# Kernel optimization log

Hardware: AMD Instinct MI355X
Metric: run time of the kernel (lower is better)

Reference implementation:

```python
import jax, jax.numpy as jnp
import numpy as np

BIG = 1e8  # > max possible squared distance in a 64^3 volume (3*63^2 ~ 1.2e4)


def _edt(mask):
    """Exact Euclidean distance transform (scipy.ndimage.distance_transform_edt).

    mask: [B, X, Y, Z] float; distance at nonzero voxels to nearest zero voxel.
    Uses the exact separable squared-EDT: along each axis,
      g[i] = min_j f[j] + (i - j)^2  (lower envelope of parabolas, brute-forced).
    """
    f = jnp.where(mask > 0, BIG, 0.0).astype(jnp.float32)
    for ax in (1, 2, 3):
        f = jnp.moveaxis(f, ax, -1)            # [..., n]
        n = f.shape[-1]
        i = jnp.arange(n)
        d2 = ((i[:, None] - i[None, :]) ** 2).astype(jnp.float32)  # [n, n]
        f = jnp.min(f[..., None, :] + d2, axis=-1)                 # [..., n]
        f = jnp.moveaxis(f, -1, ax)
    return jnp.sqrt(f)


def _get_dist_map(mmap, label_inner, label_outer):
    lz = jnp.isin(mmap, jnp.asarray(label_outer)).astype(jnp.float32)
    lz = jnp.where(jnp.isin(mmap, jnp.asarray(label_inner)), 0.0, lz)
    tdm_outer = _edt(lz)                       # distance inside outer region to its zero set
    b = _edt(1.0 - lz)
    boundary = jnp.where(b == 1.0, 1.0, 0.0)   # boundary[boundary != 1] = 0
    outer = tdm_outer + boundary
    level_zero_inner = (outer == 0.0).astype(jnp.float32)
    tsd = -_edt(level_zero_inner) + tdm_outer  # signed distance
    return boundary, tsd


def setup_inputs() -> dict:
    key = jax.random.key(0)
    mmap = jax.random.randint(key, (2, 64, 64, 64), 0, 10, dtype=jnp.int32)
    return {"mmap": mmap}


def reference(mmap):
    d_mean = 2.0
    inner_boundary, phi_inner = _get_dist_map(mmap, [3, 5, 6, 7, 8, 9], [2, 1, 4, 0])
    outer_boundary, phi_outer = _get_dist_map(mmap, [3, 5, 6, 7, 8, 9, 2], [1, 4, 0])
    hausdorff_inner = jnp.abs(inner_boundary * phi_outer)
    hausdorff_outer = jnp.abs(outer_boundary * phi_inner)
    h_in_mean = hausdorff_inner.sum() / inner_boundary.sum()
    h_out_mean = hausdorff_outer.sum() / outer_boundary.sum()
    loss = (h_in_mean - d_mean) ** 2 + (h_out_mean - d_mean) ** 2
    return (h_in_mean, hausdorff_inner.max(), h_out_mean, hausdorff_outer.max(), loss)
```

## Files before the change

### kernel.cpp

```cpp
#include <hip/hip_runtime.h>
#include <hip/hip_bf16.h>
#include <math.h>

#define N 64
#define BATCH 2
#define PLANE (N * N)
#define VOL (BATCH * N * N * N)
#define BIGF 1e8f
#define LP 65
#define FBIG 3.4e38f
#define MASK1 0x17u
#define MASK2 0x13u


#define BITS_OFF ((size_t)8 * VOL)
#define PART_OFF (BITS_OFF + (size_t)2 * BATCH * N * N * 8)
#define CNT_OFF (PART_OFF + (size_t)256 * 8 * 4)

__global__ __launch_bounds__(512) void edt_yz(const int* __restrict__ mmap,
                                              void* __restrict__ wsv) {
  __shared__ unsigned char colb[3][8][64];
  __shared__ unsigned long long colm[3][64];
  __shared__ unsigned long long zmT[64];
  __shared__ unsigned long long zmL[64];
  __shared__ float Bm1[N][LP];
  __shared__ float Bm2[N][LP];
  const int m = blockIdx.x >> 7;
  const int plane = blockIdx.x & 127;
  const int b = plane >> 6, x = plane & 63;
  const int t = threadIdx.x;
  const int z = t & 63, c = t >> 6;
  const unsigned lmask = m ? MASK2 : MASK1;
  const size_t bbase = (size_t)(b * N) * PLANE;

  if (blockIdx.x == 0 && t == 0) *(int*)((char*)wsv + CNT_OFF) = 0;

  #pragma unroll
  for (int p = 0; p < 3; ++p) {
    const int xp = x + p - 1;
    unsigned byte = 0;
    if (xp >= 0 && xp < N) {
      const size_t pb = bbase + (size_t)xp * PLANE;
      #pragma unroll
      for (int k = 0; k < 8; ++k) {
        const int y = 8 * c + k;
        byte |= ((lmask >> mmap[pb + y * N + z]) & 1u) << k;
      }
    }
    colb[p][c][z] = (unsigned char)byte;
  }
  __syncthreads();
  if (t < 192) {
    const int p = t >> 6, zz = t & 63;
    unsigned long long v = 0;
    #pragma unroll
    for (int cc = 0; cc < 8; ++cc)
      v |= (unsigned long long)colb[p][cc][zz] << (8 * cc);
    colm[p][zz] = v;
  }
  __syncthreads();
  if (t < 64) {
    const unsigned long long cx = colm[1][t];
    unsigned long long nb = colm[0][t] | colm[2][t] | (cx << 1) | (cx >> 1);
    if (t > 0) nb |= colm[1][t - 1];
    if (t < 63) nb |= colm[1][t + 1];
    zmT[t] = ~cx;
    zmL[t] = cx | nb;
    unsigned long long* bits =
        (unsigned long long*)((char*)wsv + BITS_OFF) + (size_t)m * (BATCH * N * N);
    bits[(size_t)(b * N + x) * N + t] = nb & ~cx;
  }
  __syncthreads();

  {
    const unsigned long long M0 = zmT[z];
    const unsigned long long M1 = zmL[z];
    const float zs = (float)(z * z);
    #pragma unroll
    for (int k = 0; k < 8; ++k) {
      const int y = 8 * c + k;
      {
        const unsigned long long lo = M0 << (63 - y);
        const int dl = __clzll((long long)lo);
        const int f = __ffsll((long long)(M0 >> y));
        const int d = min(dl, f ? (f - 1) : 99);
        Bm1[y][z] = (d > 63) ? BIGF : (float)(d * d) + zs;
      }
      {
        const unsigned long long lo = M1 << (63 - y);
        const int dl = __clzll((long long)lo);
        const int f = __ffsll((long long)(M1 >> y));
        const int d = min(dl, f ? (f - 1) : 99);
        Bm2[y][z] = (d > 63) ? BIGF : (float)(d * d) + zs;
      }
    }
  }
  __syncthreads();

  const int y = t & 63, w = t >> 6;
  float a1[8], a2[8], zq[8];
  #pragma unroll
  for (int q = 0; q < 8; ++q) { a1[q] = FBIG; a2[q] = FBIG; zq[q] = (float)(w + 8 * q); }
  float m2j = 0.f;
  #pragma unroll 2
  for (int j = 0; j < N; ++j) {
    const float f1 = Bm1[y][j];
    const float f2 = Bm2[y][j];
    #pragma unroll
    for (int q = 0; q < 8; ++q) {
      a1[q] = fminf(a1[q], fmaf(m2j, zq[q], f1));
      a2[q] = fminf(a2[q], fmaf(m2j, zq[q], f2));
    }
    m2j -= 2.f;
  }
  __syncthreads();
  #pragma unroll
  for (int q = 0; q < 8; ++q) {
    Bm1[y][w + 8 * q] = fmaf(zq[q], zq[q], a1[q]);
    Bm2[y][w + 8 * q] = fmaf(zq[q], zq[q], a2[q]);
  }
  __syncthreads();
  unsigned short* mid1 = (unsigned short*)wsv + (size_t)m * VOL;
  unsigned short* mid2 = (unsigned short*)wsv + (size_t)(2 + m) * VOL;
  const size_t pbase = (size_t)(b * N + x) * PLANE;
  #pragma unroll
  for (int k = 0; k < 8; ++k) {
    const int e = t + 512 * k;
    mid1[pbase + e] = (unsigned short)fminf(Bm1[e >> 6][e & 63], 65535.f);
    mid2[pbase + e] = (unsigned short)fminf(Bm2[e >> 6][e & 63], 65535.f);
  }
}

__global__ __launch_bounds__(512) void edt_x_fused(void* __restrict__ wsv,
                                                   float* __restrict__ out) {
  __shared__ float A1[N][LP];
  __shared__ float A2[N][LP];
  __shared__ float redS[8], redM[8], redB[8];
  __shared__ int lastFlag;
  const int m = blockIdx.x >> 7;
  const int plane = blockIdx.x & 127;
  const int b = plane >> 6, y = plane & 63;
  const int t = threadIdx.x;
  const int z = t & 63, w = t >> 6;

  const unsigned short* mid1 = (const unsigned short*)wsv + (size_t)m * VOL;
  const unsigned short* mid2 = (const unsigned short*)wsv + (size_t)(2 + m) * VOL;
  #pragma unroll
  for (int k = 0; k < 8; ++k) {
    const int e = t + 512 * k;
    const int xx = e >> 6, zz = e & 63;
    const float xs = (float)(xx * xx);
    const size_t idx = (size_t)(b * N + xx) * PLANE + y * N + zz;
    const unsigned v1 = mid1[idx];
    const unsigned v2 = mid2[idx];
    A1[xx][zz] = ((v1 == 65535u) ? BIGF : (float)v1) + xs;
    A2[xx][zz] = ((v2 == 65535u) ? BIGF : (float)v2) + xs;
  }
  __syncthreads();

  float a1[8], a2[8], xq[8];
  #pragma unroll
  for (int q = 0; q < 8; ++q) { a1[q] = FBIG; a2[q] = FBIG; xq[q] = (float)(w + 8 * q); }
  float m2j = 0.f;
  #pragma unroll 2
  for (int j = 0; j < N; ++j) {
    const float f1 = A1[j][z];
    const float f2 = A2[j][z];
    #pragma unroll
    for (int q = 0; q < 8; ++q) {
      a1[q] = fminf(a1[q], fmaf(m2j, xq[q], f1));
      a2[q] = fminf(a2[q], fmaf(m2j, xq[q], f2));
    }
    m2j -= 2.f;
  }

  const unsigned long long* bits =
      (const unsigned long long*)((char*)wsv + BITS_OFF) +
      (size_t)(m == 0 ? 1 : 0) * (BATCH * N * N);
  float hsum = 0.f, hmax = 0.f, bsum = 0.f;
  #pragma unroll
  for (int q = 0; q < 8; ++q) {
    const float e1 = fmaf(xq[q], xq[q], a1[q]);
    const float e2 = fmaf(xq[q], xq[q], a2[q]);
    const float tsd = sqrtf(e1) - sqrtf(e2);
    const int xx = w + 8 * q;
    const unsigned long long bv = bits[(size_t)(b * N + xx) * N + z];
    const float bnd = (float)((bv >> y) & 1ull);
    const float h = bnd * fabsf(tsd);
    hsum += h; bsum += bnd; hmax = fmaxf(hmax, h);
  }
  #pragma unroll
  for (int o = 32; o > 0; o >>= 1) {
    hsum += __shfl_down(hsum, o);
    bsum += __shfl_down(bsum, o);
    hmax = fmaxf(hmax, __shfl_down(hmax, o));
  }
  if (z == 0) { redS[w] = hsum; redB[w] = bsum; redM[w] = hmax; }
  __syncthreads();

  float* part = (float*)((char*)wsv + PART_OFF);
  int* cnt = (int*)((char*)wsv + CNT_OFF);
  if (t == 0) {
    float s = 0.f, bs = 0.f, mx = 0.f;
    #pragma unroll
    for (int i = 0; i < 8; ++i) {
      s += redS[i]; bs += redB[i]; mx = fmaxf(mx, redM[i]);
    }
    float* p = part + (size_t)blockIdx.x * 8;
    p[0] = s; p[1] = bs; p[2] = mx;
    __threadfence();
    const int old = atomicAdd(cnt, 1);
    lastFlag = (old == 255) ? 1 : 0;
  }
  __syncthreads();
  if (lastFlag) {
    __threadfence();
    float s = 0.f, bs = 0.f, mx = 0.f;
    if (t < 256) {
      const float* p = part + (size_t)t * 8;
      s = p[0]; bs = p[1]; mx = p[2];
    }
    #pragma unroll
    for (int o = 32; o > 0; o >>= 1) {
      s += __shfl_down(s, o);
      bs += __shfl_down(bs, o);
      mx = fmaxf(mx, __shfl_down(mx, o));
    }
    __syncthreads();
    if ((t & 63) == 0 && t < 256) {
      redS[t >> 6] = s; redB[t >> 6] = bs; redM[t >> 6] = mx;
    }
    __syncthreads();
    if (t == 0) {
      const float s_ho = redS[0] + redS[1], b2 = redB[0] + redB[1];
      const float mho = fmaxf(redM[0], redM[1]);
      const float s_hi = redS[2] + redS[3], b1 = redB[2] + redB[3];
      const float mhi = fmaxf(redM[2], redM[3]);
      const float him = s_hi / b1;
      const float hom = s_ho / b2;
      out[0] = him;
      out[1] = mhi;
      out[2] = hom;
      out[3] = mho;
      out[4] = (him - 2.f) * (him - 2.f) + (hom - 2.f) * (hom - 2.f);
    }
  }
}

extern "C" void kernel_launch(void* const* d_in, const int* in_sizes, int n_in,
                              void* d_out, int out_size, void* d_ws,
                              size_t ws_size, hipStream_t stream) {
  (void)in_sizes; (void)n_in; (void)out_size; (void)ws_size;
  const int* mmap = (const int*)d_in[0];
  float* out = (float*)d_out;

  edt_yz<<<2 * BATCH * N, 512, 0, stream>>>(mmap, d_ws);
  edt_x_fused<<<2 * BATCH * N, 512, 0, stream>>>(d_ws, out);
}
```

Measured before the change: 31.74 us.

## Double threads per block and vectorize LDS reads with float4 rows

Both kernels now run 1024 threads per block instead of 512, halving per-thread work (4 outputs per thread instead of 8) and adjusting the bit-packing, reduction arrays and store loops to match. The x-pass shared tile is stored transposed so each thread reads its own row, and both min-plus loops read shared memory as 128-bit float4 vectors with the row pitch padded to 68 for alignment. The aim is more parallelism across only 256 blocks and fewer LDS load instructions. The cost is possible bank conflicts from the transposed writes and row-wise vector reads, plus higher register pressure at 1024 threads.

New measurement: 32.66 us. +2.9%, slower.

```diff
diff --git a/kernel.cpp b/kernel.cpp
--- a/kernel.cpp
+++ b/kernel.cpp
@@ -7,7 +7,7 @@
 #define PLANE (N * N)
 #define VOL (BATCH * N * N * N)
 #define BIGF 1e8f
-#define LP 65
+#define LP 68
 #define FBIG 3.4e38f
 #define MASK1 0x17u
 #define MASK2 0x13u
@@ -17,9 +17,11 @@
 #define PART_OFF (BITS_OFF + (size_t)2 * BATCH * N * N * 8)
 #define CNT_OFF (PART_OFF + (size_t)256 * 8 * 4)
 
-__global__ __launch_bounds__(512) void edt_yz(const int* __restrict__ mmap,
-                                              void* __restrict__ wsv) {
-  __shared__ unsigned char colb[3][8][64];
+typedef __attribute__((ext_vector_type(4))) float f32x4;
+
+__global__ __launch_bounds__(1024) void edt_yz(const int* __restrict__ mmap,
+                                               void* __restrict__ wsv) {
+  __shared__ unsigned char colb[3][16][64];
   __shared__ unsigned long long colm[3][64];
   __shared__ unsigned long long zmT[64];
   __shared__ unsigned long long zmL[64];
@@ -38,24 +40,24 @@
   #pragma unroll
   for (int p = 0; p < 3; ++p) {
     const int xp = x + p - 1;
-    unsigned byte = 0;
+    unsigned nib = 0;
     if (xp >= 0 && xp < N) {
       const size_t pb = bbase + (size_t)xp * PLANE;
       #pragma unroll
-      for (int k = 0; k < 8; ++k) {
-        const int y = 8 * c + k;
-        byte |= ((lmask >> mmap[pb + y * N + z]) & 1u) << k;
-      }
-    }
-    colb[p][c][z] = (unsigned char)byte;
+      for (int k = 0; k < 4; ++k) {
+        const int y = 4 * c + k;
+        nib |= ((lmask >> mmap[pb + y * N + z]) & 1u) << k;
+      }
+    }
+    colb[p][c][z] = (unsigned char)nib;
   }
   __syncthreads();
   if (t < 192) {
     const int p = t >> 6, zz = t & 63;
     unsigned long long v = 0;
     #pragma unroll
-    for (int cc = 0; cc < 8; ++cc)
-      v |= (unsigned long long)colb[p][cc][zz] << (8 * cc);
+    for (int cc = 0; cc < 16; ++cc)
+      v |= (unsigned long long)colb[p][cc][zz] << (4 * cc);
     colm[p][zz] = v;
   }
   __syncthreads();
@@ -77,8 +79,8 @@
     const unsigned long long M1 = zmL[z];
     const float zs = (float)(z * z);
     #pragma unroll
-    for (int k = 0; k < 8; ++k) {
-      const int y = 8 * c + k;
+    for (int k = 0; k < 4; ++k) {
+      const int y = 4 * c + k;
       {
         const unsigned long long lo = M0 << (63 - y);
         const int dl = __clzll((long long)lo);
@@ -98,44 +100,49 @@
   __syncthreads();
 
   const int y = t & 63, w = t >> 6;
-  float a1[8], a2[8], zq[8];
-  #pragma unroll
-  for (int q = 0; q < 8; ++q) { a1[q] = FBIG; a2[q] = FBIG; zq[q] = (float)(w + 8 * q); }
+  const f32x4* B1row = (const f32x4*)&Bm1[y][0];
+  const f32x4* B2row = (const f32x4*)&Bm2[y][0];
+  float a1[4], a2[4], zq[4];
+  #pragma unroll
+  for (int q = 0; q < 4; ++q) { a1[q] = FBIG; a2[q] = FBIG; zq[q] = (float)(w + 16 * q); }
   float m2j = 0.f;
-  #pragma unroll 2
-  for (int j = 0; j < N; ++j) {
-    const float f1 = Bm1[y][j];
-    const float f2 = Bm2[y][j];
-    #pragma unroll
-    for (int q = 0; q < 8; ++q) {
-      a1[q] = fminf(a1[q], fmaf(m2j, zq[q], f1));
-      a2[q] = fminf(a2[q], fmaf(m2j, zq[q], f2));
-    }
-    m2j -= 2.f;
-  }
-  __syncthreads();
-  #pragma unroll
-  for (int q = 0; q < 8; ++q) {
-    Bm1[y][w + 8 * q] = fmaf(zq[q], zq[q], a1[q]);
-    Bm2[y][w + 8 * q] = fmaf(zq[q], zq[q], a2[q]);
+  #pragma unroll 4
+  for (int j4 = 0; j4 < 16; ++j4) {
+    const f32x4 f1 = B1row[j4];
+    const f32x4 f2 = B2row[j4];
+    #pragma unroll
+    for (int e = 0; e < 4; ++e) {
+      #pragma unroll
+      for (int q = 0; q < 4; ++q) {
+        a1[q] = fminf(a1[q], fmaf(m2j, zq[q], f1[e]));
+        a2[q] = fminf(a2[q], fmaf(m2j, zq[q], f2[e]));
+      }
+      m2j -= 2.f;
+    }
+  }
+  __syncthreads();
+  #pragma unroll
+  for (int q = 0; q < 4; ++q) {
+    Bm1[y][w + 16 * q] = fmaf(zq[q], zq[q], a1[q]);
+    Bm2[y][w + 16 * q] = fmaf(zq[q], zq[q], a2[q]);
   }
   __syncthreads();
   unsigned short* mid1 = (unsigned short*)wsv + (size_t)m * VOL;
   unsigned short* mid2 = (unsigned short*)wsv + (size_t)(2 + m) * VOL;
   const size_t pbase = (size_t)(b * N + x) * PLANE;
   #pragma unroll
-  for (int k = 0; k < 8; ++k) {
-    const int e = t + 512 * k;
+  for (int k = 0; k < 4; ++k) {
+    const int e = t + 1024 * k;
     mid1[pbase + e] = (unsigned short)fminf(Bm1[e >> 6][e & 63], 65535.f);
     mid2[pbase + e] = (unsigned short)fminf(Bm2[e >> 6][e & 63], 65535.f);
   }
 }
 
-__global__ __launch_bounds__(512) void edt_x_fused(void* __restrict__ wsv,
-                                                   float* __restrict__ out) {
+__global__ __launch_bounds__(1024) void edt_x_fused(void* __restrict__ wsv,
+                                                    float* __restrict__ out) {
   __shared__ float A1[N][LP];
   __shared__ float A2[N][LP];
-  __shared__ float redS[8], redM[8], redB[8];
+  __shared__ float redS[16], redM[16], redB[16];
   __shared__ int lastFlag;
   const int m = blockIdx.x >> 7;
   const int plane = blockIdx.x & 127;
@@ -146,32 +153,37 @@
   const unsigned short* mid1 = (const unsigned short*)wsv + (size_t)m * VOL;
   const unsigned short* mid2 = (const unsigned short*)wsv + (size_t)(2 + m) * VOL;
   #pragma unroll
-  for (int k = 0; k < 8; ++k) {
-    const int e = t + 512 * k;
+  for (int k = 0; k < 4; ++k) {
+    const int e = t + 1024 * k;
     const int xx = e >> 6, zz = e & 63;
     const float xs = (float)(xx * xx);
     const size_t idx = (size_t)(b * N + xx) * PLANE + y * N + zz;
     const unsigned v1 = mid1[idx];
     const unsigned v2 = mid2[idx];
-    A1[xx][zz] = ((v1 == 65535u) ? BIGF : (float)v1) + xs;
-    A2[xx][zz] = ((v2 == 65535u) ? BIGF : (float)v2) + xs;
-  }
-  __syncthreads();
-
-  float a1[8], a2[8], xq[8];
-  #pragma unroll
-  for (int q = 0; q < 8; ++q) { a1[q] = FBIG; a2[q] = FBIG; xq[q] = (float)(w + 8 * q); }
+    A1[zz][xx] = ((v1 == 65535u) ? BIGF : (float)v1) + xs;
+    A2[zz][xx] = ((v2 == 65535u) ? BIGF : (float)v2) + xs;
+  }
+  __syncthreads();
+
+  const f32x4* A1row = (const f32x4*)&A1[z][0];
+  const f32x4* A2row = (const f32x4*)&A2[z][0];
+  float a1[4], a2[4], xq[4];
+  #pragma unroll
+  for (int q = 0; q < 4; ++q) { a1[q] = FBIG; a2[q] = FBIG; xq[q] = (float)(w + 16 * q); }
   float m2j = 0.f;
-  #pragma unroll 2
-  for (int j = 0; j < N; ++j) {
-    const float f1 = A1[j][z];
-    const float f2 = A2[j][z];
-    #pragma unroll
-    for (int q = 0; q < 8; ++q) {
-      a1[q] = fminf(a1[q], fmaf(m2j, xq[q], f1));
-      a2[q] = fminf(a2[q], fmaf(m2j, xq[q], f2));
-    }
-    m2j -= 2.f;
+  #pragma unroll 4
+  for (int j4 = 0; j4 < 16; ++j4) {
+    const f32x4 f1 = A1row[j4];
+    const f32x4 f2 = A2row[j4];
+    #pragma unroll
+    for (int e = 0; e < 4; ++e) {
+      #pragma unroll
+      for (int q = 0; q < 4; ++q) {
+        a1[q] = fminf(a1[q], fmaf(m2j, xq[q], f1[e]));
+        a2[q] = fminf(a2[q], fmaf(m2j, xq[q], f2[e]));
+      }
+      m2j -= 2.f;
+    }
   }
 
   const unsigned long long* bits =
@@ -179,11 +191,11 @@
       (size_t)(m == 0 ? 1 : 0) * (BATCH * N * N);
   float hsum = 0.f, hmax = 0.f, bsum = 0.f;
   #pragma unroll
-  for (int q = 0; q < 8; ++q) {
+  for (int q = 0; q < 4; ++q) {
     const float e1 = fmaf(xq[q], xq[q], a1[q]);
     const float e2 = fmaf(xq[q], xq[q], a2[q]);
     const float tsd = sqrtf(e1) - sqrtf(e2);
-    const int xx = w + 8 * q;
+    const int xx = w + 16 * q;
     const unsigned long long bv = bits[(size_t)(b * N + xx) * N + z];
     const float bnd = (float)((bv >> y) & 1ull);
     const float h = bnd * fabsf(tsd);
@@ -203,7 +215,7 @@
   if (t == 0) {
     float s = 0.f, bs = 0.f, mx = 0.f;
     #pragma unroll
-    for (int i = 0; i < 8; ++i) {
+    for (int i = 0; i < 16; ++i) {
       s += redS[i]; bs += redB[i]; mx = fmaxf(mx, redM[i]);
     }
     float* p = part + (size_t)blockIdx.x * 8;
@@ -254,6 +266,6 @@
   const int* mmap = (const int*)d_in[0];
   float* out = (float*)d_out;
 
-  edt_yz<<<2 * BATCH * N, 512, 0, stream>>>(mmap, d_ws);
-  edt_x_fused<<<2 * BATCH * N, 512, 0, stream>>>(d_ws, out);
+  edt_yz<<<2 * BATCH * N, 1024, 0, stream>>>(mmap, d_ws);
+  edt_x_fused<<<2 * BATCH * N, 1024, 0, stream>>>(d_ws, out);
 }
```

## Fuse two EDT kernels into one with a grid-wide spin barrier

Applied to the files above, without the earlier changes.

Merges the y/z EDT pass and the x pass plus reduction into a single kernel of 256 blocks that synchronises through an atomic counter and a spin-wait barrier. Counters are zeroed with a memset before launch. The aim is to remove the second kernel launch and the gap between launches. The risk is that the barrier relies on all 256 blocks being resident at once, and the added memset is its own small operation.

New measurement: 56.98 us. 1.79x slower.

```diff
diff --git a/kernel.cpp b/kernel.cpp
--- a/kernel.cpp
+++ b/kernel.cpp
@@ -15,234 +15,250 @@
 
 #define BITS_OFF ((size_t)8 * VOL)
 #define PART_OFF (BITS_OFF + (size_t)2 * BATCH * N * N * 8)
-#define CNT_OFF (PART_OFF + (size_t)256 * 8 * 4)
-
-__global__ __launch_bounds__(512) void edt_yz(const int* __restrict__ mmap,
-                                              void* __restrict__ wsv) {
+#define CTR_OFF (PART_OFF + (size_t)256 * 8 * 4)
+
+__global__ __launch_bounds__(512) void hausdorff_fused(
+    const int* __restrict__ mmap, void* __restrict__ wsv,
+    float* __restrict__ out) {
   __shared__ unsigned char colb[3][8][64];
   __shared__ unsigned long long colm[3][64];
   __shared__ unsigned long long zmT[64];
   __shared__ unsigned long long zmL[64];
   __shared__ float Bm1[N][LP];
   __shared__ float Bm2[N][LP];
-  const int m = blockIdx.x >> 7;
-  const int plane = blockIdx.x & 127;
-  const int b = plane >> 6, x = plane & 63;
+  __shared__ float redS[8], redM[8], redB[8];
+  __shared__ int lastFlag;
+
+  const int bid = blockIdx.x;
+  const int m = bid >> 7;
+  const int plane = bid & 127;
+  const int b = plane >> 6;
   const int t = threadIdx.x;
   const int z = t & 63, c = t >> 6;
   const unsigned lmask = m ? MASK2 : MASK1;
-  const size_t bbase = (size_t)(b * N) * PLANE;
-
-  if (blockIdx.x == 0 && t == 0) *(int*)((char*)wsv + CNT_OFF) = 0;
-
-  #pragma unroll
-  for (int p = 0; p < 3; ++p) {
-    const int xp = x + p - 1;
-    unsigned byte = 0;
-    if (xp >= 0 && xp < N) {
-      const size_t pb = bbase + (size_t)xp * PLANE;
+  int* ctr = (int*)((char*)wsv + CTR_OFF);
+
+  {
+    const int x = plane & 63;
+    const size_t bbase = (size_t)(b * N) * PLANE;
+
+    #pragma unroll
+    for (int p = 0; p < 3; ++p) {
+      const int xp = x + p - 1;
+      unsigned byte = 0;
+      if (xp >= 0 && xp < N) {
+        const size_t pb = bbase + (size_t)xp * PLANE;
+        #pragma unroll
+        for (int k = 0; k < 8; ++k) {
+          const int y = 8 * c + k;
+          byte |= ((lmask >> mmap[pb + y * N + z]) & 1u) << k;
+        }
+      }
+      colb[p][c][z] = (unsigned char)byte;
+    }
+    __syncthreads();
+    if (t < 192) {
+      const int p = t >> 6, zz = t & 63;
+      unsigned long long v = 0;
+      #pragma unroll
+      for (int cc = 0; cc < 8; ++cc)
+        v |= (unsigned long long)colb[p][cc][zz] << (8 * cc);
+      colm[p][zz] = v;
+    }
+    __syncthreads();
+    if (t < 64) {
+      const unsigned long long cx = colm[1][t];
+      unsigned long long nb = colm[0][t] | colm[2][t] | (cx << 1) | (cx >> 1);
+      if (t > 0) nb |= colm[1][t - 1];
+      if (t < 63) nb |= colm[1][t + 1];
+      zmT[t] = ~cx;
+      zmL[t] = cx | nb;
+      unsigned long long* bits = (unsigned long long*)((char*)wsv + BITS_OFF) +
+                                 (size_t)m * (BATCH * N * N);
+      bits[(size_t)(b * N + x) * N + t] = nb & ~cx;
+    }
+    __syncthreads();
+
+    {
+      const unsigned long long M0 = zmT[z];
+      const unsigned long long M1 = zmL[z];
+      const float zs = (float)(z * z);
       #pragma unroll
       for (int k = 0; k < 8; ++k) {
         const int y = 8 * c + k;
-        byte |= ((lmask >> mmap[pb + y * N + z]) & 1u) << k;
-      }
-    }
-    colb[p][c][z] = (unsigned char)byte;
+        {
+          const unsigned long long lo = M0 << (63 - y);
+          const int dl = __clzll((long long)lo);
+          const int f = __ffsll((long long)(M0 >> y));
+          const int d = min(dl, f ? (f - 1) : 99);
+          Bm1[y][z] = (d > 63) ? BIGF : (float)(d * d) + zs;
+        }
+        {
+          const unsigned long long lo = M1 << (63 - y);
+          const int dl = __clzll((long long)lo);
+          const int f = __ffsll((long long)(M1 >> y));
+          const int d = min(dl, f ? (f - 1) : 99);
+          Bm2[y][z] = (d > 63) ? BIGF : (float)(d * d) + zs;
+        }
+      }
+    }
+    __syncthreads();
+
+    const int y = t & 63, w = t >> 6;
+    float a1[8], a2[8], zq[8];
+    #pragma unroll
+    for (int q = 0; q < 8; ++q) {
+      a1[q] = FBIG; a2[q] = FBIG; zq[q] = (float)(w + 8 * q);
+    }
+    float m2j = 0.f;
+    #pragma unroll 2
+    for (int j = 0; j < N; ++j) {
+      const float f1 = Bm1[y][j];
+      const float f2 = Bm2[y][j];
+      #pragma unroll
+      for (int q = 0; q < 8; ++q) {
+        a1[q] = fminf(a1[q], fmaf(m2j, zq[q], f1));
+        a2[q] = fminf(a2[q], fmaf(m2j, zq[q], f2));
+      }
+      m2j -= 2.f;
+    }
+    __syncthreads();
+    #pragma unroll
+    for (int q = 0; q < 8; ++q) {
+      Bm1[y][w + 8 * q] = fmaf(zq[q], zq[q], a1[q]);
+      Bm2[y][w + 8 * q] = fmaf(zq[q], zq[q], a2[q]);
+    }
+    __syncthreads();
+    unsigned short* mid1 = (unsigned short*)wsv + (size_t)m * VOL;
+    unsigned short* mid2 = (unsigned short*)wsv + (size_t)(2 + m) * VOL;
+    const size_t pbase = (size_t)(b * N + x) * PLANE;
+    #pragma unroll
+    for (int k = 0; k < 8; ++k) {
+      const int e = t + 512 * k;
+      mid1[pbase + e] = (unsigned short)fminf(Bm1[e >> 6][e & 63], 65535.f);
+      mid2[pbase + e] = (unsigned short)fminf(Bm2[e >> 6][e & 63], 65535.f);
+    }
+  }
+
+  __syncthreads();
+  if (t == 0) {
+    __threadfence();
+    atomicAdd(&ctr[0], 1);
+    while (__hip_atomic_load(&ctr[0], __ATOMIC_ACQUIRE,
+                             __HIP_MEMORY_SCOPE_AGENT) < 256) {
+      __builtin_amdgcn_s_sleep(2);
+    }
+    __threadfence();
   }
   __syncthreads();
-  if (t < 192) {
-    const int p = t >> 6, zz = t & 63;
-    unsigned long long v = 0;
-    #pragma unroll
-    for (int cc = 0; cc < 8; ++cc)
-      v |= (unsigned long long)colb[p][cc][zz] << (8 * cc);
-    colm[p][zz] = v;
-  }
-  __syncthreads();
-  if (t < 64) {
-    const unsigned long long cx = colm[1][t];
-    unsigned long long nb = colm[0][t] | colm[2][t] | (cx << 1) | (cx >> 1);
-    if (t > 0) nb |= colm[1][t - 1];
-    if (t < 63) nb |= colm[1][t + 1];
-    zmT[t] = ~cx;
-    zmL[t] = cx | nb;
-    unsigned long long* bits =
-        (unsigned long long*)((char*)wsv + BITS_OFF) + (size_t)m * (BATCH * N * N);
-    bits[(size_t)(b * N + x) * N + t] = nb & ~cx;
-  }
-  __syncthreads();
 
   {
-    const unsigned long long M0 = zmT[z];
-    const unsigned long long M1 = zmL[z];
-    const float zs = (float)(z * z);
+    const int y = plane & 63;
+    const int w = t >> 6;
+
+    const unsigned short* mid1 = (const unsigned short*)wsv + (size_t)m * VOL;
+    const unsigned short* mid2 =
+        (const unsigned short*)wsv + (size_t)(2 + m) * VOL;
     #pragma unroll
     for (int k = 0; k < 8; ++k) {
-      const int y = 8 * c + k;
-      {
-        const unsigned long long lo = M0 << (63 - y);
-        const int dl = __clzll((long long)lo);
-        const int f = __ffsll((long long)(M0 >> y));
-        const int d = min(dl, f ? (f - 1) : 99);
-        Bm1[y][z] = (d > 63) ? BIGF : (float)(d * d) + zs;
-      }
-      {
-        const unsigned long long lo = M1 << (63 - y);
-        const int dl = __clzll((long long)lo);
-        const int f = __ffsll((long long)(M1 >> y));
-        const int d = min(dl, f ? (f - 1) : 99);
-        Bm2[y][z] = (d > 63) ? BIGF : (float)(d * d) + zs;
-      }
-    }
-  }
-  __syncthreads();
-
-  const int y = t & 63, w = t >> 6;
-  float a1[8], a2[8], zq[8];
-  #pragma unroll
-  for (int q = 0; q < 8; ++q) { a1[q] = FBIG; a2[q] = FBIG; zq[q] = (float)(w + 8 * q); }
-  float m2j = 0.f;
-  #pragma unroll 2
-  for (int j = 0; j < N; ++j) {
-    const float f1 = Bm1[y][j];
-    const float f2 = Bm2[y][j];
-    #pragma unroll
-    for (int q = 0; q < 8; ++q) {
-      a1[q] = fminf(a1[q], fmaf(m2j, zq[q], f1));
-      a2[q] = fminf(a2[q], fmaf(m2j, zq[q], f2));
-    }
-    m2j -= 2.f;
-  }
-  __syncthreads();
-  #pragma unroll
-  for (int q = 0; q < 8; ++q) {
-    Bm1[y][w + 8 * q] = fmaf(zq[q], zq[q], a1[q]);
-    Bm2[y][w + 8 * q] = fmaf(zq[q], zq[q], a2[q]);
-  }
-  __syncthreads();
-  unsigned short* mid1 = (unsigned short*)wsv + (size_t)m * VOL;
-  unsigned short* mid2 = (unsigned short*)wsv + (size_t)(2 + m) * VOL;
-  const size_t pbase = (size_t)(b * N + x) * PLANE;
-  #pragma unroll
-  for (int k = 0; k < 8; ++k) {
-    const int e = t + 512 * k;
-    mid1[pbase + e] = (unsigned short)fminf(Bm1[e >> 6][e & 63], 65535.f);
-    mid2[pbase + e] = (unsigned short)fminf(Bm2[e >> 6][e & 63], 65535.f);
-  }
-}
-
-__global__ __launch_bounds__(512) void edt_x_fused(void* __restrict__ wsv,
-                                                   float* __restrict__ out) {
-  __shared__ float A1[N][LP];
-  __shared__ float A2[N][LP];
-  __shared__ float redS[8], redM[8], redB[8];
-  __shared__ int lastFlag;
-  const int m = blockIdx.x >> 7;
-  const int plane = blockIdx.x & 127;
-  const int b = plane >> 6, y = plane & 63;
-  const int t = threadIdx.x;
-  const int z = t & 63, w = t >> 6;
-
-  const unsigned short* mid1 = (const unsigned short*)wsv + (size_t)m * VOL;
-  const unsigned short* mid2 = (const unsigned short*)wsv + (size_t)(2 + m) * VOL;
-  #pragma unroll
-  for (int k = 0; k < 8; ++k) {
-    const int e = t + 512 * k;
-    const int xx = e >> 6, zz = e & 63;
-    const float xs = (float)(xx * xx);
-    const size_t idx = (size_t)(b * N + xx) * PLANE + y * N + zz;
-    const unsigned v1 = mid1[idx];
-    const unsigned v2 = mid2[idx];
-    A1[xx][zz] = ((v1 == 65535u) ? BIGF : (float)v1) + xs;
-    A2[xx][zz] = ((v2 == 65535u) ? BIGF : (float)v2) + xs;
-  }
-  __syncthreads();
-
-  float a1[8], a2[8], xq[8];
-  #pragma unroll
-  for (int q = 0; q < 8; ++q) { a1[q] = FBIG; a2[q] = FBIG; xq[q] = (float)(w + 8 * q); }
-  float m2j = 0.f;
-  #pragma unroll 2
-  for (int j = 0; j < N; ++j) {
-    const float f1 = A1[j][z];
-    const float f2 = A2[j][z];
-    #pragma unroll
-    for (int q = 0; q < 8; ++q) {
-      a1[q] = fminf(a1[q], fmaf(m2j, xq[q], f1));
-      a2[q] = fminf(a2[q], fmaf(m2j, xq[q], f2));
-    }
-    m2j -= 2.f;
-  }
-
-  const unsigned long long* bits =
-      (const unsigned long long*)((char*)wsv + BITS_OFF) +
-      (size_t)(m == 0 ? 1 : 0) * (BATCH * N * N);
-  float hsum = 0.f, hmax = 0.f, bsum = 0.f;
-  #pragma unroll
-  for (int q = 0; q < 8; ++q) {
-    const float e1 = fmaf(xq[q], xq[q], a1[q]);
-    const float e2 = fmaf(xq[q], xq[q], a2[q]);
-    const float tsd = sqrtf(e1) - sqrtf(e2);
-    const int xx = w + 8 * q;
-    const unsigned long long bv = bits[(size_t)(b * N + xx) * N + z];
-    const float bnd = (float)((bv >> y) & 1ull);
-    const float h = bnd * fabsf(tsd);
-    hsum += h; bsum += bnd; hmax = fmaxf(hmax, h);
-  }
-  #pragma unroll
-  for (int o = 32; o > 0; o >>= 1) {
-    hsum += __shfl_down(hsum, o);
-    bsum += __shfl_down(bsum, o);
-    hmax = fmaxf(hmax, __shfl_down(hmax, o));
-  }
-  if (z == 0) { redS[w] = hsum; redB[w] = bsum; redM[w] = hmax; }
-  __syncthreads();
-
-  float* part = (float*)((char*)wsv + PART_OFF);
-  int* cnt = (int*)((char*)wsv + CNT_OFF);
-  if (t == 0) {
-    float s = 0.f, bs = 0.f, mx = 0.f;
-    #pragma unroll
-    for (int i = 0; i < 8; ++i) {
-      s += redS[i]; bs += redB[i]; mx = fmaxf(mx, redM[i]);
-    }
-    float* p = part + (size_t)blockIdx.x * 8;
-    p[0] = s; p[1] = bs; p[2] = mx;
-    __threadfence();
-    const int old = atomicAdd(cnt, 1);
-    lastFlag = (old == 255) ? 1 : 0;
-  }
-  __syncthreads();
-  if (lastFlag) {
-    __threadfence();
-    float s = 0.f, bs = 0.f, mx = 0.f;
-    if (t < 256) {
-      const float* p = part + (size_t)t * 8;
-      s = p[0]; bs = p[1]; mx = p[2];
+      const int e = t + 512 * k;
+      const int xx = e >> 6, zz = e & 63;
+      const float xs = (float)(xx * xx);
+      const size_t idx = (size_t)(b * N + xx) * PLANE + y * N + zz;
+      const unsigned v1 = mid1[idx];
+      const unsigned v2 = mid2[idx];
+      Bm1[xx][zz] = ((v1 == 65535u) ? BIGF : (float)v1) + xs;
+      Bm2[xx][zz] = ((v2 == 65535u) ? BIGF : (float)v2) + xs;
+    }
+    __syncthreads();
+
+    float a1[8], a2[8], xq[8];
+    #pragma unroll
+    for (int q = 0; q < 8; ++q) {
+      a1[q] = FBIG; a2[q] = FBIG; xq[q] = (float)(w + 8 * q);
+    }
+    float m2j = 0.f;
+    #pragma unroll 2
+    for (int j = 0; j < N; ++j) {
+      const float f1 = Bm1[j][z];
+      const float f2 = Bm2[j][z];
+      #pragma unroll
+      for (int q = 0; q < 8; ++q) {
+        a1[q] = fminf(a1[q], fmaf(m2j, xq[q], f1));
+        a2[q] = fminf(a2[q], fmaf(m2j, xq[q], f2));
+      }
+      m2j -= 2.f;
+    }
+
+    const unsigned long long* bits =
+        (const unsigned long long*)((char*)wsv + BITS_OFF) +
+        (size_t)(m == 0 ? 1 : 0) * (BATCH * N * N);
+    float hsum = 0.f, hmax = 0.f, bsum = 0.f;
+    #pragma unroll
+    for (int q = 0; q < 8; ++q) {
+      const float e1 = fmaf(xq[q], xq[q], a1[q]);
+      const float e2 = fmaf(xq[q], xq[q], a2[q]);
+      const float tsd = sqrtf(e1) - sqrtf(e2);
+      const int xx = w + 8 * q;
+      const unsigned long long bv = bits[(size_t)(b * N + xx) * N + z];
+      const float bnd = (float)((bv >> y) & 1ull);
+      const float h = bnd * fabsf(tsd);
+      hsum += h; bsum += bnd; hmax = fmaxf(hmax, h);
     }
     #pragma unroll
     for (int o = 32; o > 0; o >>= 1) {
-      s += __shfl_down(s, o);
-      bs += __shfl_down(bs, o);
-      mx = fmaxf(mx, __shfl_down(mx, o));
-    }
-    __syncthreads();
-    if ((t & 63) == 0 && t < 256) {
-      redS[t >> 6] = s; redB[t >> 6] = bs; redM[t >> 6] = mx;
-    }
-    __syncthreads();
+      hsum += __shfl_down(hsum, o);
+      bsum += __shfl_down(bsum, o);
+      hmax = fmaxf(hmax, __shfl_down(hmax, o));
+    }
+    if (z == 0) { redS[w] = hsum; redB[w] = bsum; redM[w] = hmax; }
+    __syncthreads();
+
+    float* part = (float*)((char*)wsv + PART_OFF);
     if (t == 0) {
-      const float s_ho = redS[0] + redS[1], b2 = redB[0] + redB[1];
-      const float mho = fmaxf(redM[0], redM[1]);
-      const float s_hi = redS[2] + redS[3], b1 = redB[2] + redB[3];
-      const float mhi = fmaxf(redM[2], redM[3]);
-      const float him = s_hi / b1;
-      const float hom = s_ho / b2;
-      out[0] = him;
-      out[1] = mhi;
-      out[2] = hom;
-      out[3] = mho;
-      out[4] = (him - 2.f) * (him - 2.f) + (hom - 2.f) * (hom - 2.f);
+      float s = 0.f, bs = 0.f, mx = 0.f;
+      #pragma unroll
+      for (int i = 0; i < 8; ++i) {
+        s += redS[i]; bs += redB[i]; mx = fmaxf(mx, redM[i]);
+      }
+      float* p = part + (size_t)bid * 8;
+      p[0] = s; p[1] = bs; p[2] = mx;
+      __threadfence();
+      const int old = atomicAdd(&ctr[1], 1);
+      lastFlag = (old == 255) ? 1 : 0;
+    }
+    __syncthreads();
+    if (lastFlag) {
+      __threadfence();
+      float s = 0.f, bs = 0.f, mx = 0.f;
+      if (t < 256) {
+        const float* p = part + (size_t)t * 8;
+        s = p[0]; bs = p[1]; mx = p[2];
+      }
+      #pragma unroll
+      for (int o = 32; o > 0; o >>= 1) {
+        s += __shfl_down(s, o);
+        bs += __shfl_down(bs, o);
+        mx = fmaxf(mx, __shfl_down(mx, o));
+      }
+      __syncthreads();
+      if ((t & 63) == 0 && t < 256) {
+        redS[t >> 6] = s; redB[t >> 6] = bs; redM[t >> 6] = mx;
+      }
+      __syncthreads();
+      if (t == 0) {
+        const float s_ho = redS[0] + redS[1], b2 = redB[0] + redB[1];
+        const float mho = fmaxf(redM[0], redM[1]);
+        const float s_hi = redS[2] + redS[3], b1 = redB[2] + redB[3];
+        const float mhi = fmaxf(redM[2], redM[3]);
+        const float him = s_hi / b1;
+        const float hom = s_ho / b2;
+        out[0] = him;
+        out[1] = mhi;
+        out[2] = hom;
+        out[3] = mho;
+        out[4] = (him - 2.f) * (him - 2.f) + (hom - 2.f) * (hom - 2.f);
+      }
     }
   }
 }
@@ -254,6 +270,6 @@
   const int* mmap = (const int*)d_in[0];
   float* out = (float*)d_out;
 
-  edt_yz<<<2 * BATCH * N, 512, 0, stream>>>(mmap, d_ws);
-  edt_x_fused<<<2 * BATCH * N, 512, 0, stream>>>(d_ws, out);
+  hipMemsetAsync((char*)d_ws + CTR_OFF, 0, 8, stream);
+  hausdorff_fused<<<2 * BATCH * N, 512, 0, stream>>>(mmap, d_ws, out);
 }
```
